# Kernel tuning notes

Measured on AMD Instinct MI355X. Metric: run time of the kernel, lower is better.

Reference implementation:

```python
import jax, jax.numpy as jnp
import numpy as np

QUALITY = 95
X_MIN, X_MAX = 0.0, 1.0

# JPEG Annex K base quantization tables
_LUMA = np.array([
    [16, 11, 10, 16, 24, 40, 51, 61],
    [12, 12, 14, 19, 26, 58, 60, 55],
    [14, 13, 16, 24, 40, 57, 69, 56],
    [14, 17, 22, 29, 51, 87, 80, 62],
    [18, 22, 37, 56, 68, 109, 103, 77],
    [24, 35, 55, 64, 81, 104, 113, 92],
    [49, 64, 78, 87, 103, 121, 120, 101],
    [72, 92, 95, 98, 112, 100, 103, 99]], dtype=np.float32)
_CHROMA = np.array([
    [17, 18, 24, 47, 99, 99, 99, 99],
    [18, 21, 26, 66, 99, 99, 99, 99],
    [24, 26, 56, 99, 99, 99, 99, 99],
    [47, 66, 99, 99, 99, 99, 99, 99],
    [99, 99, 99, 99, 99, 99, 99, 99],
    [99, 99, 99, 99, 99, 99, 99, 99],
    [99, 99, 99, 99, 99, 99, 99, 99],
    [99, 99, 99, 99, 99, 99, 99, 99]], dtype=np.float32)

def _qtable(base, quality):
    # libjpeg quality scaling (quality >= 50 branch)
    scale = 5000.0 / quality if quality < 50 else 200.0 - 2.0 * quality
    return np.clip(np.floor((base * scale + 50.0) / 100.0), 1.0, 255.0).astype(np.float32)

_QL = jnp.asarray(_qtable(_LUMA, QUALITY))
_QC = jnp.asarray(_qtable(_CHROMA, QUALITY))

# Orthonormal 8x8 DCT-II matrix
_k = np.arange(8)
_D = np.sqrt(2.0 / 8.0) * np.cos((2 * _k[None, :] + 1) * _k[:, None] * np.pi / 16.0)
_D[0, :] /= np.sqrt(2.0)
_D = jnp.asarray(_D.astype(np.float32))

def _jpeg_channel(ch, table):
    """8x8 block DCT -> quantize(round) -> dequantize -> IDCT. ch: [B,H,W] level-shifted."""
    B, H, W = ch.shape
    xb = ch.reshape(B, H // 8, 8, W // 8, 8)
    coef = jnp.einsum('ki,bhiwj,lj->bhkwl', _D, xb, _D)
    t = table[None, None, :, None, :]
    deq = jnp.round(coef / t) * t
    rec = jnp.einsum('ki,bhkwl,lj->bhiwj', _D, deq, _D)
    return rec.reshape(B, H, W)

def _jpeg_roundtrip(x255):
    """x255: [B,H,W,3] float values in [0,255]. Simulates JPEG encode+decode (4:2:0)."""
    r, g, b = x255[..., 0], x255[..., 1], x255[..., 2]
    # JFIF RGB -> YCbCr
    y = 0.299 * r + 0.587 * g + 0.114 * b
    cb = -0.168736 * r - 0.331264 * g + 0.5 * b + 128.0
    cr = 0.5 * r - 0.418688 * g - 0.081312 * b + 128.0
    # Luma at full resolution
    y2 = _jpeg_channel(y - 128.0, _QL) + 128.0
    # Chroma: 2x2 average downsample (4:2:0), codec, nearest upsample
    def down(c):
        B, H, W = c.shape
        return c.reshape(B, H // 2, 2, W // 2, 2).mean(axis=(2, 4))
    def up(c):
        return jnp.repeat(jnp.repeat(c, 2, axis=1), 2, axis=2)
    cb2 = up(_jpeg_channel(down(cb) - 128.0, _QC) + 128.0)
    cr2 = up(_jpeg_channel(down(cr) - 128.0, _QC) + 128.0)
    # YCbCr -> RGB
    r2 = y2 + 1.402 * (cr2 - 128.0)
    g2 = y2 - 0.344136 * (cb2 - 128.0) - 0.714136 * (cr2 - 128.0)
    b2 = y2 + 1.772 * (cb2 - 128.0)
    rgb = jnp.stack([r2, g2, b2], axis=-1)
    return jnp.round(jnp.clip(rgb, 0.0, 255.0))  # decoded uint8 values


def setup_inputs() -> dict:
    key = jax.random.key(0)
    x = jax.random.uniform(key, (32, 512, 512, 3), dtype=jnp.float32)
    return {"x": x}


def reference(x):
    # inputs -> uint8 pixel values (tf.cast truncation; values are >= 0)
    x255 = jnp.clip(jnp.floor((x - X_MIN) / ((X_MAX - X_MIN) / 255.0)), 0.0, 255.0)
    dec = _jpeg_roundtrip(x255)
    # back to input range/dtype
    return dec / (255.0 / (X_MAX - X_MIN)) + X_MIN
```

## Files before the change

kernel.cpp:

```cpp
#include <hip/hip_runtime.h>
#include <cstddef>

static constexpr float D8[8][8] = {
  { 0.35355339059327373f, 0.35355339059327373f, 0.35355339059327373f, 0.35355339059327373f,
    0.35355339059327373f, 0.35355339059327373f, 0.35355339059327373f, 0.35355339059327373f},
  { 0.4903926402016152f,  0.4157348061512726f,  0.27778511650980114f, 0.09754516100806417f,
   -0.09754516100806417f,-0.27778511650980114f,-0.4157348061512726f, -0.4903926402016152f},
  { 0.46193976625564337f, 0.19134171618254492f,-0.19134171618254492f,-0.46193976625564337f,
   -0.46193976625564337f,-0.19134171618254492f, 0.19134171618254492f, 0.46193976625564337f},
  { 0.4157348061512726f, -0.09754516100806417f,-0.4903926402016152f, -0.27778511650980114f,
    0.27778511650980114f, 0.4903926402016152f,  0.09754516100806417f,-0.4157348061512726f},
  { 0.35355339059327373f,-0.35355339059327373f,-0.35355339059327373f, 0.35355339059327373f,
    0.35355339059327373f,-0.35355339059327373f,-0.35355339059327373f, 0.35355339059327373f},
  { 0.27778511650980114f,-0.4903926402016152f,  0.09754516100806417f, 0.4157348061512726f,
   -0.4157348061512726f, -0.09754516100806417f, 0.4903926402016152f, -0.27778511650980114f},
  { 0.19134171618254492f,-0.46193976625564337f, 0.46193976625564337f,-0.19134171618254492f,
   -0.19134171618254492f, 0.46193976625564337f,-0.46193976625564337f, 0.19134171618254492f},
  { 0.09754516100806417f,-0.27778511650980114f, 0.4157348061512726f, -0.4903926402016152f,
    0.4903926402016152f, -0.4157348061512726f,  0.27778511650980114f,-0.09754516100806417f},
};

static constexpr float QLt[8][8] = {
  {2,1,1,2,2,4,5,6},
  {1,1,1,2,3,6,6,6},
  {1,1,2,2,4,6,7,6},
  {1,2,2,3,5,9,8,6},
  {2,2,4,6,7,11,10,8},
  {2,4,6,6,8,10,11,9},
  {5,6,8,9,10,12,12,10},
  {7,9,10,10,11,10,10,10},
};
static constexpr float QCt[8][8] = {
  {2,2,2,5,10,10,10,10},
  {2,2,3,7,10,10,10,10},
  {2,3,6,10,10,10,10,10},
  {5,7,10,10,10,10,10,10},
  {10,10,10,10,10,10,10,10},
  {10,10,10,10,10,10,10,10},
  {10,10,10,10,10,10,10,10},
  {10,10,10,10,10,10,10,10},
};

struct QE { double r; float q; float pad; };
struct QTabE { QE v[8][8]; };
static constexpr QTabE mkqe(const float (&b)[8][8]) {
  QTabE t{};
  for (int i = 0; i < 8; ++i)
    for (int j = 0; j < 8; ++j)
      t.v[i][j] = QE{1.0 / (double)b[i][j], b[i][j], 0.0f};
  return t;
}
static constexpr QTabE QLe = mkqe(QLt);
static constexpr QTabE QCe = mkqe(QCt);

__device__ __forceinline__ void dct8(const float x[8], float u[8]) {
  #pragma unroll
  for (int k = 0; k < 8; ++k) {
    float a = D8[k][0] * x[0];
    #pragma unroll
    for (int j = 1; j < 8; ++j) a += D8[k][j] * x[j];
    u[k] = a;
  }
}
__device__ __forceinline__ void idct8(const float x[8], float u[8]) {
  #pragma unroll
  for (int j = 0; j < 8; ++j) {
    float a = x[0] * D8[0][j];
    #pragma unroll
    for (int m = 1; m < 8; ++m) a += x[m] * D8[m][j];
    u[j] = a;
  }
}

__device__ __forceinline__ float to255(float x) {
  constexpr double R = 1.0 / (double)(1.0f / 255.0f);
  float q = (float)((double)x * R);
  return fminf(fmaxf(floorf(q), 0.0f), 255.0f);
}

__device__ __forceinline__ float quant_rt(float u, const QE& e) {
  float t = (float)((double)u * e.r);
  return rintf(t) * e.q;
}

__global__ __launch_bounds__(128, 8) void jpeg_rt(const float* __restrict__ in,
                                                  float* __restrict__ out)
{
  __shared__ __align__(16) float LDSB[2 * 896];

  const int t   = threadIdx.x;
  const int w   = t >> 6;
  const int l   = t & 63;
  const int tx  = blockIdx.x;
  const int ty  = blockIdx.y;
  const int img = blockIdx.z;

  float* P = LDSB + w * 896;

  const int pr = l >> 3;
  const int pc = l & 7;
  const int colbase = tx*64 + w*32 + 4*pc;

  {
    const size_t r0 = (size_t)img * 512 + (size_t)(ty*16 + 2*pr);
    const float* rp0 = in + (r0*512 + colbase)*3;
    const float* rp1 = rp0 + 512*3;
    float4 L0 = ((const float4*)rp0)[0];
    float4 L1 = ((const float4*)rp0)[1];
    float4 L2 = ((const float4*)rp0)[2];
    float4 L3 = ((const float4*)rp1)[0];
    float4 L4 = ((const float4*)rp1)[1];
    float4 L5 = ((const float4*)rp1)[2];
    float px[2][12] = {{L0.x,L0.y,L0.z,L0.w,L1.x,L1.y,L1.z,L1.w,L2.x,L2.y,L2.z,L2.w},
                       {L3.x,L3.y,L3.z,L3.w,L4.x,L4.y,L4.z,L4.w,L5.x,L5.y,L5.z,L5.w}};
    float yv[2][4], cbv[2][4], crv[2][4];
    #pragma unroll
    for (int rr = 0; rr < 2; ++rr) {
      #pragma unroll
      for (int p = 0; p < 4; ++p) {
        float r = to255(px[rr][3*p+0]);
        float g = to255(px[rr][3*p+1]);
        float b = to255(px[rr][3*p+2]);
        float y  =  0.299f*r + 0.587f*g + 0.114f*b;
        float cb = -0.168736f*r - 0.331264f*g + 0.5f*b + 128.0f;
        float cr =  0.5f*r - 0.418688f*g - 0.081312f*b + 128.0f;
        yv[rr][p]  = y - 128.0f;
        cbv[rr][p] = cb;
        crv[rr][p] = cr;
      }
    }
    *(float4*)&P[(2*pr+0)*36 + 4*pc] = make_float4(yv[0][0],yv[0][1],yv[0][2],yv[0][3]);
    *(float4*)&P[(2*pr+1)*36 + 4*pc] = make_float4(yv[1][0],yv[1][1],yv[1][2],yv[1][3]);
    float cb0 = ((cbv[0][0]+cbv[0][1]) + (cbv[1][0]+cbv[1][1]))*0.25f - 128.0f;
    float cb1 = ((cbv[0][2]+cbv[0][3]) + (cbv[1][2]+cbv[1][3]))*0.25f - 128.0f;
    float cr0 = ((crv[0][0]+crv[0][1]) + (crv[1][0]+crv[1][1]))*0.25f - 128.0f;
    float cr1 = ((crv[0][2]+crv[0][3]) + (crv[1][2]+crv[1][3]))*0.25f - 128.0f;
    *(float2*)&P[576 + pr*20 + 2*pc] = make_float2(cb0, cb1);
    *(float2*)&P[736 + pr*20 + 2*pc] = make_float2(cr0, cr1);
  }

  auto planeAddr = [](int tb, int i) -> int {
    if (tb < 8)  return ((tb >> 2)*8 + i)*36 + (tb & 3)*8;
    if (tb < 10) return 576 + i*20 + (tb - 8)*8;
    return 736 + i*20 + (tb - 10)*8;
  };

  const int tb0 = l >> 3;
  const int tb1 = 8 + (l >> 3);
  const int ri  = l & 7;

  {
    float xr[8], u[8];
    const float* src = P + planeAddr(tb0, ri);
    *(float4*)&xr[0] = *(const float4*)&src[0];
    *(float4*)&xr[4] = *(const float4*)&src[4];
    dct8(xr, u);
    *(float4*)&P[tb0*68 + ri*8 + 0] = make_float4(u[0],u[1],u[2],u[3]);
    *(float4*)&P[tb0*68 + ri*8 + 4] = make_float4(u[4],u[5],u[6],u[7]);
    if (l < 32) {
      const float* src1 = P + planeAddr(tb1, ri);
      *(float4*)&xr[0] = *(const float4*)&src1[0];
      *(float4*)&xr[4] = *(const float4*)&src1[4];
      dct8(xr, u);
      *(float4*)&P[tb1*68 + ri*8 + 0] = make_float4(u[0],u[1],u[2],u[3]);
      *(float4*)&P[tb1*68 + ri*8 + 4] = make_float4(u[4],u[5],u[6],u[7]);
    }
  }

  {
    float s[8], u[8], v[8];
    #pragma unroll
    for (int i = 0; i < 8; ++i) s[i] = P[tb0*68 + i*8 + ri];
    dct8(s, u);
    #pragma unroll
    for (int m = 0; m < 8; ++m) u[m] = quant_rt(u[m], QLe.v[m][ri]);
    idct8(u, v);
    *(float4*)&P[tb0*68 + ri*8 + 0] = make_float4(v[0],v[1],v[2],v[3]);
    *(float4*)&P[tb0*68 + ri*8 + 4] = make_float4(v[4],v[5],v[6],v[7]);
    if (l < 32) {
      #pragma unroll
      for (int i = 0; i < 8; ++i) s[i] = P[tb1*68 + i*8 + ri];
      dct8(s, u);
      #pragma unroll
      for (int m = 0; m < 8; ++m) u[m] = quant_rt(u[m], QCe.v[m][ri]);
      idct8(u, v);
      *(float4*)&P[tb1*68 + ri*8 + 0] = make_float4(v[0],v[1],v[2],v[3]);
      *(float4*)&P[tb1*68 + ri*8 + 4] = make_float4(v[4],v[5],v[6],v[7]);
    }
  }

  {
    float w0[8], w1[8], z[8];
    #pragma unroll
    for (int m = 0; m < 8; ++m) w0[m] = P[tb0*68 + m*8 + ri];
    if (l < 32) {
      #pragma unroll
      for (int m = 0; m < 8; ++m) w1[m] = P[tb1*68 + m*8 + ri];
    }
    idct8(w0, z);
    float* dst = P + planeAddr(tb0, ri);
    *(float4*)&dst[0] = make_float4(z[0],z[1],z[2],z[3]);
    *(float4*)&dst[4] = make_float4(z[4],z[5],z[6],z[7]);
    if (l < 32) {
      idct8(w1, z);
      float* dst1 = P + planeAddr(tb1, ri);
      *(float4*)&dst1[0] = make_float4(z[0],z[1],z[2],z[3]);
      *(float4*)&dst1[4] = make_float4(z[4],z[5],z[6],z[7]);
    }
  }

  {
    const float c255 = (float)(1.0 / 255.0);
    float y0[4], y1[4];
    *(float4*)y0 = *(const float4*)&P[(2*pr+0)*36 + 4*pc];
    *(float4*)y1 = *(const float4*)&P[(2*pr+1)*36 + 4*pc];
    float2 cbp2 = *(const float2*)&P[576 + pr*20 + 2*pc];
    float2 crp2 = *(const float2*)&P[736 + pr*20 + 2*pc];
    float cbq[2] = {cbp2.x, cbp2.y};
    float crq[2] = {crp2.x, crp2.y};
    #pragma unroll
    for (int rr = 0; rr < 2; ++rr) {
      float ov[12];
      #pragma unroll
      for (int p = 0; p < 4; ++p) {
        float y2  = (rr ? y1[p] : y0[p]) + 128.0f;
        float cb2 = cbq[p>>1] + 128.0f;
        float cr2 = crq[p>>1] + 128.0f;
        float r2 = y2 + 1.402f*(cr2 - 128.0f);
        float g2 = y2 - 0.344136f*(cb2 - 128.0f) - 0.714136f*(cr2 - 128.0f);
        float b2 = y2 + 1.772f*(cb2 - 128.0f);
        ov[3*p+0] = rintf(fminf(fmaxf(r2, 0.0f), 255.0f)) * c255;
        ov[3*p+1] = rintf(fminf(fmaxf(g2, 0.0f), 255.0f)) * c255;
        ov[3*p+2] = rintf(fminf(fmaxf(b2, 0.0f), 255.0f)) * c255;
      }
      const size_t grow = (size_t)img * 512 + (size_t)(ty*16 + 2*pr + rr);
      float* op = out + (grow*512 + colbase)*3;
      ((float4*)op)[0] = make_float4(ov[0],ov[1],ov[2],ov[3]);
      ((float4*)op)[1] = make_float4(ov[4],ov[5],ov[6],ov[7]);
      ((float4*)op)[2] = make_float4(ov[8],ov[9],ov[10],ov[11]);
    }
  }
}

extern "C" void kernel_launch(void* const* d_in, const int* in_sizes, int n_in,
                              void* d_out, int out_size, void* d_ws, size_t ws_size,
                              hipStream_t stream) {
  (void)in_sizes; (void)n_in; (void)d_ws; (void)ws_size; (void)out_size;
  const float* x = (const float*)d_in[0];
  float* out = (float*)d_out;
  dim3 grid(8, 32, 32);
  jpeg_rt<<<grid, dim3(128), 0, stream>>>(x, out);
}
```

Baseline: 186.2 us.

## Process a whole 8x8 luma block per thread in registers

Each thread now owns one full 8x8 luma block, doing both DCT passes, quantization and IDCT in registers instead of staging through LDS across lanes. Chroma blocks are downsampled into LDS and then processed whole by half of the wave. The block shrinks to one 64-thread wavefront covering a 32x128 tile. The aim is to cut LDS traffic and cross-lane shuffling, at the cost of very high register pressure, lower occupancy, poorly coalesced strided global accesses and idle lanes during the chroma stage.

```diff
diff --git a/kernel.cpp b/kernel.cpp
--- a/kernel.cpp
+++ b/kernel.cpp
@@ -83,161 +83,155 @@
   return rintf(t) * e.q;
 }
 
-__global__ __launch_bounds__(128, 8) void jpeg_rt(const float* __restrict__ in,
-                                                  float* __restrict__ out)
+__device__ __forceinline__ void dct_block(float (&y)[64], const QTabE& Q) {
+  float t[8], u[8];
+  #pragma unroll
+  for (int i = 0; i < 8; ++i) {
+    #pragma unroll
+    for (int j = 0; j < 8; ++j) t[j] = y[i*8+j];
+    dct8(t, u);
+    #pragma unroll
+    for (int j = 0; j < 8; ++j) y[i*8+j] = u[j];
+  }
+  #pragma unroll
+  for (int b = 0; b < 8; ++b) {
+    #pragma unroll
+    for (int i = 0; i < 8; ++i) t[i] = y[i*8+b];
+    dct8(t, u);
+    #pragma unroll
+    for (int m = 0; m < 8; ++m) u[m] = quant_rt(u[m], Q.v[m][b]);
+    idct8(u, t);
+    #pragma unroll
+    for (int i = 0; i < 8; ++i) y[i*8+b] = t[i];
+  }
+  #pragma unroll
+  for (int i = 0; i < 8; ++i) {
+    #pragma unroll
+    for (int j = 0; j < 8; ++j) t[j] = y[i*8+j];
+    idct8(t, u);
+    #pragma unroll
+    for (int j = 0; j < 8; ++j) y[i*8+j] = u[j];
+  }
+}
+
+__global__ __launch_bounds__(64, 2) void jpeg_rt(const float* __restrict__ in,
+                                                 float* __restrict__ out)
 {
-  __shared__ __align__(16) float LDSB[2 * 896];
-
-  const int t   = threadIdx.x;
-  const int w   = t >> 6;
-  const int l   = t & 63;
+  __shared__ __align__(16) float CH[2304];
+
+  const int l   = threadIdx.x;
   const int tx  = blockIdx.x;
   const int ty  = blockIdx.y;
   const int img = blockIdx.z;
 
-  float* P = LDSB + w * 896;
-
-  const int pr = l >> 3;
-  const int pc = l & 7;
-  const int colbase = tx*64 + w*32 + 4*pc;
+  const int bc = l & 15, br = l >> 4;
+  const int row0 = ty*32 + br*8;
+  const int col0 = tx*128 + bc*8;
+  const int mbi = (br >> 1)*8 + (bc >> 1);
+  const int qr  = br & 1, qc = bc & 1;
+
+  const float* gbase = in + ((size_t)(img*512 + row0)*512 + col0)*3;
+
+  float y[64];
 
   {
-    const size_t r0 = (size_t)img * 512 + (size_t)(ty*16 + 2*pr);
-    const float* rp0 = in + (r0*512 + colbase)*3;
-    const float* rp1 = rp0 + 512*3;
-    float4 L0 = ((const float4*)rp0)[0];
-    float4 L1 = ((const float4*)rp0)[1];
-    float4 L2 = ((const float4*)rp0)[2];
-    float4 L3 = ((const float4*)rp1)[0];
-    float4 L4 = ((const float4*)rp1)[1];
-    float4 L5 = ((const float4*)rp1)[2];
-    float px[2][12] = {{L0.x,L0.y,L0.z,L0.w,L1.x,L1.y,L1.z,L1.w,L2.x,L2.y,L2.z,L2.w},
-                       {L3.x,L3.y,L3.z,L3.w,L4.x,L4.y,L4.z,L4.w,L5.x,L5.y,L5.z,L5.w}};
-    float yv[2][4], cbv[2][4], crv[2][4];
-    #pragma unroll
-    for (int rr = 0; rr < 2; ++rr) {
+    float cbA[8], crA[8];
+    #pragma unroll
+    for (int rp = 0; rp < 4; ++rp) {
       #pragma unroll
-      for (int p = 0; p < 4; ++p) {
-        float r = to255(px[rr][3*p+0]);
-        float g = to255(px[rr][3*p+1]);
-        float b = to255(px[rr][3*p+2]);
-        float y  =  0.299f*r + 0.587f*g + 0.114f*b;
-        float cb = -0.168736f*r - 0.331264f*g + 0.5f*b + 128.0f;
-        float cr =  0.5f*r - 0.418688f*g - 0.081312f*b + 128.0f;
-        yv[rr][p]  = y - 128.0f;
-        cbv[rr][p] = cb;
-        crv[rr][p] = cr;
+      for (int h = 0; h < 2; ++h) {
+        const int r = rp*2 + h;
+        const float* rpx = gbase + (size_t)r*1536;
+        float4 L0 = ((const float4*)rpx)[0];
+        float4 L1 = ((const float4*)rpx)[1];
+        float4 L2 = ((const float4*)rpx)[2];
+        float4 L3 = ((const float4*)rpx)[3];
+        float4 L4 = ((const float4*)rpx)[4];
+        float4 L5 = ((const float4*)rpx)[5];
+        float px[24] = {L0.x,L0.y,L0.z,L0.w, L1.x,L1.y,L1.z,L1.w,
+                        L2.x,L2.y,L2.z,L2.w, L3.x,L3.y,L3.z,L3.w,
+                        L4.x,L4.y,L4.z,L4.w, L5.x,L5.y,L5.z,L5.w};
+        float cbr[8], crr[8];
+        #pragma unroll
+        for (int p = 0; p < 8; ++p) {
+          float R = to255(px[3*p+0]);
+          float G = to255(px[3*p+1]);
+          float B = to255(px[3*p+2]);
+          float Y = 0.299f*R + 0.587f*G + 0.114f*B;
+          y[r*8+p] = Y - 128.0f;
+          cbr[p] = -0.168736f*R - 0.331264f*G + 0.5f*B + 128.0f;
+          crr[p] =  0.5f*R - 0.418688f*G - 0.081312f*B + 128.0f;
+        }
+        if (h == 0) {
+          #pragma unroll
+          for (int p = 0; p < 8; ++p) { cbA[p] = cbr[p]; crA[p] = crr[p]; }
+        } else {
+          float pb[4], pr2[4];
+          #pragma unroll
+          for (int c = 0; c < 4; ++c) {
+            pb[c]  = ((cbA[2*c]+cbA[2*c+1]) + (cbr[2*c]+cbr[2*c+1]))*0.25f - 128.0f;
+            pr2[c] = ((crA[2*c]+crA[2*c+1]) + (crr[2*c]+crr[2*c+1]))*0.25f - 128.0f;
+          }
+          *(float4*)&CH[       mbi*72 + (qr*4+rp)*8 + qc*4] = make_float4(pb[0],pb[1],pb[2],pb[3]);
+          *(float4*)&CH[1152 + mbi*72 + (qr*4+rp)*8 + qc*4] = make_float4(pr2[0],pr2[1],pr2[2],pr2[3]);
+        }
       }
     }
-    *(float4*)&P[(2*pr+0)*36 + 4*pc] = make_float4(yv[0][0],yv[0][1],yv[0][2],yv[0][3]);
-    *(float4*)&P[(2*pr+1)*36 + 4*pc] = make_float4(yv[1][0],yv[1][1],yv[1][2],yv[1][3]);
-    float cb0 = ((cbv[0][0]+cbv[0][1]) + (cbv[1][0]+cbv[1][1]))*0.25f - 128.0f;
-    float cb1 = ((cbv[0][2]+cbv[0][3]) + (cbv[1][2]+cbv[1][3]))*0.25f - 128.0f;
-    float cr0 = ((crv[0][0]+crv[0][1]) + (crv[1][0]+crv[1][1]))*0.25f - 128.0f;
-    float cr1 = ((crv[0][2]+crv[0][3]) + (crv[1][2]+crv[1][3]))*0.25f - 128.0f;
-    *(float2*)&P[576 + pr*20 + 2*pc] = make_float2(cb0, cb1);
-    *(float2*)&P[736 + pr*20 + 2*pc] = make_float2(cr0, cr1);
-  }
-
-  auto planeAddr = [](int tb, int i) -> int {
-    if (tb < 8)  return ((tb >> 2)*8 + i)*36 + (tb & 3)*8;
-    if (tb < 10) return 576 + i*20 + (tb - 8)*8;
-    return 736 + i*20 + (tb - 10)*8;
-  };
-
-  const int tb0 = l >> 3;
-  const int tb1 = 8 + (l >> 3);
-  const int ri  = l & 7;
-
-  {
-    float xr[8], u[8];
-    const float* src = P + planeAddr(tb0, ri);
-    *(float4*)&xr[0] = *(const float4*)&src[0];
-    *(float4*)&xr[4] = *(const float4*)&src[4];
-    dct8(xr, u);
-    *(float4*)&P[tb0*68 + ri*8 + 0] = make_float4(u[0],u[1],u[2],u[3]);
-    *(float4*)&P[tb0*68 + ri*8 + 4] = make_float4(u[4],u[5],u[6],u[7]);
-    if (l < 32) {
-      const float* src1 = P + planeAddr(tb1, ri);
-      *(float4*)&xr[0] = *(const float4*)&src1[0];
-      *(float4*)&xr[4] = *(const float4*)&src1[4];
-      dct8(xr, u);
-      *(float4*)&P[tb1*68 + ri*8 + 0] = make_float4(u[0],u[1],u[2],u[3]);
-      *(float4*)&P[tb1*68 + ri*8 + 4] = make_float4(u[4],u[5],u[6],u[7]);
-    }
-  }
-
-  {
-    float s[8], u[8], v[8];
-    #pragma unroll
-    for (int i = 0; i < 8; ++i) s[i] = P[tb0*68 + i*8 + ri];
-    dct8(s, u);
-    #pragma unroll
-    for (int m = 0; m < 8; ++m) u[m] = quant_rt(u[m], QLe.v[m][ri]);
-    idct8(u, v);
-    *(float4*)&P[tb0*68 + ri*8 + 0] = make_float4(v[0],v[1],v[2],v[3]);
-    *(float4*)&P[tb0*68 + ri*8 + 4] = make_float4(v[4],v[5],v[6],v[7]);
-    if (l < 32) {
-      #pragma unroll
-      for (int i = 0; i < 8; ++i) s[i] = P[tb1*68 + i*8 + ri];
-      dct8(s, u);
-      #pragma unroll
-      for (int m = 0; m < 8; ++m) u[m] = quant_rt(u[m], QCe.v[m][ri]);
-      idct8(u, v);
-      *(float4*)&P[tb1*68 + ri*8 + 0] = make_float4(v[0],v[1],v[2],v[3]);
-      *(float4*)&P[tb1*68 + ri*8 + 4] = make_float4(v[4],v[5],v[6],v[7]);
-    }
-  }
-
-  {
-    float w0[8], w1[8], z[8];
-    #pragma unroll
-    for (int m = 0; m < 8; ++m) w0[m] = P[tb0*68 + m*8 + ri];
-    if (l < 32) {
-      #pragma unroll
-      for (int m = 0; m < 8; ++m) w1[m] = P[tb1*68 + m*8 + ri];
-    }
-    idct8(w0, z);
-    float* dst = P + planeAddr(tb0, ri);
-    *(float4*)&dst[0] = make_float4(z[0],z[1],z[2],z[3]);
-    *(float4*)&dst[4] = make_float4(z[4],z[5],z[6],z[7]);
-    if (l < 32) {
-      idct8(w1, z);
-      float* dst1 = P + planeAddr(tb1, ri);
-      *(float4*)&dst1[0] = make_float4(z[0],z[1],z[2],z[3]);
-      *(float4*)&dst1[4] = make_float4(z[4],z[5],z[6],z[7]);
+  }
+
+  dct_block(y, QLe);
+
+  if (l < 32) {
+    const int ch = l >> 4;
+    const int mb = l & 15;
+    const int cbase = ch*1152 + mb*72;
+    float c[64];
+    #pragma unroll
+    for (int k = 0; k < 8; ++k) {
+      *(float4*)&c[k*8+0] = *(const float4*)&CH[cbase + k*8 + 0];
+      *(float4*)&c[k*8+4] = *(const float4*)&CH[cbase + k*8 + 4];
+    }
+    dct_block(c, QCe);
+    #pragma unroll
+    for (int k = 0; k < 8; ++k) {
+      *(float4*)&CH[cbase + k*8 + 0] = *(const float4*)&c[k*8+0];
+      *(float4*)&CH[cbase + k*8 + 4] = *(const float4*)&c[k*8+4];
     }
   }
 
   {
     const float c255 = (float)(1.0 / 255.0);
-    float y0[4], y1[4];
-    *(float4*)y0 = *(const float4*)&P[(2*pr+0)*36 + 4*pc];
-    *(float4*)y1 = *(const float4*)&P[(2*pr+1)*36 + 4*pc];
-    float2 cbp2 = *(const float2*)&P[576 + pr*20 + 2*pc];
-    float2 crp2 = *(const float2*)&P[736 + pr*20 + 2*pc];
-    float cbq[2] = {cbp2.x, cbp2.y};
-    float crq[2] = {crp2.x, crp2.y};
-    #pragma unroll
-    for (int rr = 0; rr < 2; ++rr) {
-      float ov[12];
+    float* obase = out + ((size_t)(img*512 + row0)*512 + col0)*3;
+    #pragma unroll
+    for (int k = 0; k < 4; ++k) {
+      float4 cb4 = *(const float4*)&CH[       mbi*72 + (qr*4+k)*8 + qc*4];
+      float4 cr4 = *(const float4*)&CH[1152 + mbi*72 + (qr*4+k)*8 + qc*4];
+      float cbq[4] = {cb4.x, cb4.y, cb4.z, cb4.w};
+      float crq[4] = {cr4.x, cr4.y, cr4.z, cr4.w};
       #pragma unroll
-      for (int p = 0; p < 4; ++p) {
-        float y2  = (rr ? y1[p] : y0[p]) + 128.0f;
-        float cb2 = cbq[p>>1] + 128.0f;
-        float cr2 = crq[p>>1] + 128.0f;
-        float r2 = y2 + 1.402f*(cr2 - 128.0f);
-        float g2 = y2 - 0.344136f*(cb2 - 128.0f) - 0.714136f*(cr2 - 128.0f);
-        float b2 = y2 + 1.772f*(cb2 - 128.0f);
-        ov[3*p+0] = rintf(fminf(fmaxf(r2, 0.0f), 255.0f)) * c255;
-        ov[3*p+1] = rintf(fminf(fmaxf(g2, 0.0f), 255.0f)) * c255;
-        ov[3*p+2] = rintf(fminf(fmaxf(b2, 0.0f), 255.0f)) * c255;
+      for (int h = 0; h < 2; ++h) {
+        const int r = 2*k + h;
+        float ov[24];
+        #pragma unroll
+        for (int p = 0; p < 8; ++p) {
+          float y2  = y[r*8+p] + 128.0f;
+          float cb2 = cbq[p>>1] + 128.0f;
+          float cr2 = crq[p>>1] + 128.0f;
+          float r2 = y2 + 1.402f*(cr2 - 128.0f);
+          float g2 = y2 - 0.344136f*(cb2 - 128.0f) - 0.714136f*(cr2 - 128.0f);
+          float b2 = y2 + 1.772f*(cb2 - 128.0f);
+          ov[3*p+0] = rintf(fminf(fmaxf(r2, 0.0f), 255.0f)) * c255;
+          ov[3*p+1] = rintf(fminf(fmaxf(g2, 0.0f), 255.0f)) * c255;
+          ov[3*p+2] = rintf(fminf(fmaxf(b2, 0.0f), 255.0f)) * c255;
+        }
+        float* op = obase + (size_t)r*1536;
+        ((float4*)op)[0] = make_float4(ov[0], ov[1], ov[2], ov[3]);
+        ((float4*)op)[1] = make_float4(ov[4], ov[5], ov[6], ov[7]);
+        ((float4*)op)[2] = make_float4(ov[8], ov[9], ov[10], ov[11]);
+        ((float4*)op)[3] = make_float4(ov[12],ov[13],ov[14],ov[15]);
+        ((float4*)op)[4] = make_float4(ov[16],ov[17],ov[18],ov[19]);
+        ((float4*)op)[5] = make_float4(ov[20],ov[21],ov[22],ov[23]);
       }
-      const size_t grow = (size_t)img * 512 + (size_t)(ty*16 + 2*pr + rr);
-      float* op = out + (grow*512 + colbase)*3;
-      ((float4*)op)[0] = make_float4(ov[0],ov[1],ov[2],ov[3]);
-      ((float4*)op)[1] = make_float4(ov[4],ov[5],ov[6],ov[7]);
-      ((float4*)op)[2] = make_float4(ov[8],ov[9],ov[10],ov[11]);
     }
   }
 }
@@ -248,6 +242,6 @@
   (void)in_sizes; (void)n_in; (void)d_ws; (void)ws_size; (void)out_size;
   const float* x = (const float*)d_in[0];
   float* out = (float*)d_out;
-  dim3 grid(8, 32, 32);
-  jpeg_rt<<<grid, dim3(128), 0, stream>>>(x, out);
-}
+  dim3 grid(4, 16, 32);
+  jpeg_rt<<<grid, dim3(64), 0, stream>>>(x, out);
+}
```

Measured after the change: 233.9 us. +25.6%, slower.
